# Kernel optimization log

Hardware: AMD Instinct MI355X
Metric: run time of the kernel (lower is better)

Reference implementation:

```python
import jax, jax.numpy as jnp
import numpy as np

DIM = 1024
HEAD_SIZE = 128
B, N = 4, 4096

def setup_inputs() -> dict:
    key = jax.random.key(0)
    kx, kq, kk, kv = jax.random.split(key, 4)
    s = (1.0 / DIM) ** 0.5  # ~ torch Linear init scale
    return {
        "x": jax.random.normal(kx, (B, N, DIM), dtype=jnp.float32),
        "Wq": jax.random.uniform(kq, (HEAD_SIZE, DIM), dtype=jnp.float32, minval=-s, maxval=s),
        "Wk": jax.random.uniform(kk, (HEAD_SIZE, DIM), dtype=jnp.float32, minval=-s, maxval=s),
        "Wv": jax.random.uniform(kv, (HEAD_SIZE, DIM), dtype=jnp.float32, minval=-s, maxval=s),
    }

def reference(x, Wq, Wk, Wv):
    # x: [B, N, dim]; W*: [head_size, dim] (torch Linear convention y = x @ W.T)
    q = jnp.einsum('bnd,hd->bnh', x, Wq)
    k = jnp.einsum('bnd,hd->bnh', x, Wk)
    v = jnp.einsum('bnd,hd->bnh', x, Wv)
    scale = DIM ** (-0.5)  # NOTE: original scales by dim**-0.5, not head_size
    scores = jnp.einsum('bnh,bmh->bnm', q, k) * scale  # [B, N, N]
    weights = jax.nn.softmax(scores, axis=-1)
    context = jnp.einsum('bnm,bmh->bnh', weights, v)  # [B, N, head_size]
    return context
```

## Files before the change

### kernel.cpp

```cpp
#include <hip/hip_runtime.h>

using bf16x8   = __attribute__((ext_vector_type(8))) __bf16;
using f32x4    = __attribute__((ext_vector_type(4))) float;
using f32x16   = __attribute__((ext_vector_type(16))) float;
using floatv4  = __attribute__((ext_vector_type(4))) float;
using ushortv4 = __attribute__((ext_vector_type(4))) unsigned short;
using ushortv8 = __attribute__((ext_vector_type(8))) unsigned short;
using uintv4   = __attribute__((ext_vector_type(4))) unsigned int;

#define N_SEQ 4096
#define N_B   4
#define DIMK  1024
#define HS    128
#define ROWS  (N_B * N_SEQ)
#define KVB   32
#define TT    (N_SEQ / KVB)
#define CEXPF 0.045084220027780106f

__device__ __forceinline__ unsigned short f2bf(float f) {
    unsigned u = __builtin_bit_cast(unsigned, f);
    u += 0x7FFFu + ((u >> 16) & 1u);
    return (unsigned short)(u >> 16);
}

__device__ __forceinline__ unsigned cvtpk(float lo, float hi) {
    unsigned r;
    asm("v_cvt_pk_bf16_f32 %0, %1, %2" : "=v"(r) : "v"(lo), "v"(hi));
    return r;
}

__device__ __forceinline__ void gload16(const unsigned short* g, unsigned short* l) {
    __builtin_amdgcn_global_load_lds(
        (const __attribute__((address_space(1))) unsigned int*)g,
        (__attribute__((address_space(3))) unsigned int*)l, 16, 0, 0);
}

__global__ __launch_bounds__(256) void castw_kernel(
    const float* __restrict__ Wq,
    const float* __restrict__ Wk,
    const float* __restrict__ Wv,
    unsigned short* __restrict__ Wb)
{
    const int blk = blockIdx.x;
    const int z = blk >> 6;
    const float* src = (z == 0) ? Wq : (z == 1) ? Wk : Wv;
    unsigned short* dst = Wb + (size_t)z * (HS * DIMK);
    size_t i = (size_t)(blk & 63) * 2048 + (size_t)threadIdx.x * 8;
    floatv4 a = *reinterpret_cast<const floatv4*>(src + i);
    floatv4 b = *reinterpret_cast<const floatv4*>(src + i + 4);
    ushortv8 o = { f2bf(a.x), f2bf(a.y), f2bf(a.z), f2bf(a.w),
                   f2bf(b.x), f2bf(b.y), f2bf(b.z), f2bf(b.w) };
    *reinterpret_cast<ushortv8*>(dst + i) = o;
}

__global__ __launch_bounds__(256, 3) void proj_kernel(
    const float* __restrict__ X,
    const unsigned short* __restrict__ Wb,
    unsigned short* __restrict__ Qb,
    unsigned short* __restrict__ Kb,
    unsigned short* __restrict__ Vt)
{
    const int z = blockIdx.y;
    const unsigned short* __restrict__ Wz = Wb + (size_t)z * (HS * DIMK);
    const int row0 = blockIdx.x * 64;
    __shared__ unsigned short smem[2 * 64 * 64 + 2 * 128 * 64];
    unsigned short* Xs0 = smem;
    unsigned short* Ws0 = smem + 2 * 64 * 64;
    const int tid = threadIdx.x;
    const int wv = tid >> 6, lane = tid & 63;
    const int lr = lane & 15, lg = lane >> 4;

    const int xrow = tid >> 2, xc = (tid & 3) * 16;
    const float* xg = X + (size_t)(row0 + xrow) * DIMK + xc;
    const int xs0 = (tid & 3) * 2;
    floatv4 xr[4];

    f32x4 acc[4][2] = {};

    auto loadX = [&](int k0) {
        #pragma unroll
        for (int i = 0; i < 4; ++i)
            xr[i] = *reinterpret_cast<const floatv4*>(xg + k0 + i * 4);
    };
    auto writeX = [&](int buf) {
        uintv4 w0 = { cvtpk(xr[0].x, xr[0].y), cvtpk(xr[0].z, xr[0].w),
                      cvtpk(xr[1].x, xr[1].y), cvtpk(xr[1].z, xr[1].w) };
        uintv4 w1 = { cvtpk(xr[2].x, xr[2].y), cvtpk(xr[2].z, xr[2].w),
                      cvtpk(xr[3].x, xr[3].y), cvtpk(xr[3].z, xr[3].w) };
        unsigned short* xb = Xs0 + buf * (64 * 64) + xrow * 64;
        *reinterpret_cast<uintv4*>(&xb[((xs0 ^ (xrow & 7)) * 8)]) = w0;
        *reinterpret_cast<uintv4*>(&xb[(((xs0 + 1) ^ (xrow & 7)) * 8)]) = w1;
    };
    auto stageW = [&](int buf, int k0) {
        #pragma unroll
        for (int i = 0; i < 4; ++i) {
            int g = wv * 4 + i;
            int r = g * 8 + (lane >> 3);
            int sp = (lane & 7) ^ (r & 7);
            gload16(Wz + (size_t)r * DIMK + k0 + sp * 8,
                    Ws0 + buf * (128 * 64) + g * 8 * 64);
        }
    };

    loadX(0);
    stageW(0, 0);
    asm volatile("s_waitcnt vmcnt(0)" ::: "memory");
    writeX(0);
    __syncthreads();

    for (int ks = 0; ks < DIMK / 64; ++ks) {
        const int cur = ks & 1;
        const bool more = (ks + 1 < DIMK / 64);
        if (more) { loadX((ks + 1) * 64); stageW(cur ^ 1, (ks + 1) * 64); }

        const unsigned short* Xc = Xs0 + cur * (64 * 64);
        const unsigned short* Wc = Ws0 + cur * (128 * 64);
        bf16x8 af[4][2], bfr[2][2];
        #pragma unroll
        for (int mi = 0; mi < 4; ++mi)
            #pragma unroll
            for (int kk = 0; kk < 2; ++kk)
                af[mi][kk] = *reinterpret_cast<const bf16x8*>(
                    &Xc[(mi * 16 + lr) * 64 + (((kk * 4 + lg) ^ (lr & 7)) * 8)]);
        #pragma unroll
        for (int ni = 0; ni < 2; ++ni)
            #pragma unroll
            for (int kk = 0; kk < 2; ++kk)
                bfr[ni][kk] = *reinterpret_cast<const bf16x8*>(
                    &Wc[(wv * 32 + ni * 16 + lr) * 64 + (((kk * 4 + lg) ^ (lr & 7)) * 8)]);
        #pragma unroll
        for (int kk = 0; kk < 2; ++kk)
            #pragma unroll
            for (int mi = 0; mi < 4; ++mi)
                #pragma unroll
                for (int ni = 0; ni < 2; ++ni)
                    acc[mi][ni] = __builtin_amdgcn_mfma_f32_16x16x32_bf16(
                        af[mi][kk], bfr[ni][kk], acc[mi][ni], 0, 0, 0);

        if (more) {
            asm volatile("s_waitcnt vmcnt(0)" ::: "memory");
            writeX(cur ^ 1);
        }
        __syncthreads();
    }

    if (z < 2) {
        unsigned short* O = (z == 0) ? Qb : Kb;
        const float qs = (z == 0) ? CEXPF : 1.0f;
        #pragma unroll
        for (int mi = 0; mi < 4; ++mi) {
            int rowb = row0 + mi * 16 + lg * 4;
            #pragma unroll
            for (int ni = 0; ni < 2; ++ni) {
                int col = wv * 32 + ni * 16 + lr;
                #pragma unroll
                for (int r = 0; r < 4; ++r)
                    O[(size_t)(rowb + r) * HS + col] = f2bf(acc[mi][ni][r] * qs);
            }
        }
    } else {
        unsigned short* Cs = smem;
        #pragma unroll
        for (int mi = 0; mi < 4; ++mi)
            #pragma unroll
            for (int ni = 0; ni < 2; ++ni)
                #pragma unroll
                for (int r = 0; r < 4; ++r)
                    Cs[(mi * 16 + lg * 4 + r) * 136 + wv * 32 + ni * 16 + lr] = f2bf(acc[mi][ni][r]);
        __syncthreads();
        const int b  = row0 >> 12;
        const int n0 = row0 & (N_SEQ - 1);
        #pragma unroll
        for (int i = 0; i < 2; ++i) {
            int idx = tid + i * 256;
            int d = idx >> 2, c8 = idx & 3;
            ushortv8 v;
            #pragma unroll
            for (int j = 0; j < 8; ++j)
                v[j] = Cs[(c8 * 8 + j) * 136 + d];
            *reinterpret_cast<ushortv8*>(Vt + (size_t)b * HS * N_SEQ + (size_t)d * N_SEQ + n0 + c8 * 8) = v;
        }
        #pragma unroll
        for (int i = 0; i < 2; ++i) {
            int idx = tid + i * 256;
            int d = idx >> 2, c8 = (idx & 3) + 4;
            ushortv8 v;
            #pragma unroll
            for (int j = 0; j < 8; ++j)
                v[j] = Cs[(c8 * 8 + j) * 136 + d];
            *reinterpret_cast<ushortv8*>(Vt + (size_t)b * HS * N_SEQ + (size_t)d * N_SEQ + n0 + c8 * 8) = v;
        }
    }
}

__global__ __launch_bounds__(256, 3) void attn_kernel(
    const unsigned short* __restrict__ Qb,
    const unsigned short* __restrict__ Kb,
    const unsigned short* __restrict__ Vt,
    unsigned short* __restrict__ part,
    float* __restrict__ plsum,
    int S)
{
    int qblk, split;
    {
        const int bid = blockIdx.x;
        if (S == 6) {
            const int chunk = bid >> 8, rem = bid & 255;
            const int member = rem >> 3, xcd = rem & 7;
            const int g = chunk * 8 + xcd;
            const int b = g / 6;
            split = g - b * 6;
            qblk = b * 32 + member;
        } else {
            qblk = bid & 127;
            split = bid >> 7;
        }
    }
    const int tid = threadIdx.x;
    const int wv = tid >> 6, lane = tid & 63;
    const int l31 = lane & 31, h = lane >> 5;
    const int b    = qblk >> 5;
    const int row0 = (qblk & 31) * 128 + wv * 32;

    __shared__ unsigned short Ks[3][KVB * 128];
    __shared__ unsigned short Vs[3][128 * KVB];

    bf16x8 qf[8];
    {
        const unsigned short* qp = Qb + ((size_t)b * N_SEQ + row0 + l31) * HS + h * 8;
        #pragma unroll
        for (int kk = 0; kk < 8; ++kk)
            qf[kk] = *reinterpret_cast<const bf16x8*>(qp + kk * 16);
    }

    const int base = TT / S, rem = TT % S;
    const int nt = base + (split < rem ? 1 : 0);
    const int kv_begin = (split * base + (split < rem ? split : rem)) * KVB;

    const unsigned short* Kbb = Kb + (size_t)b * N_SEQ * HS;
    const unsigned short* Vbb = Vt + (size_t)b * HS * N_SEQ;

    auto stage = [&](int buf, int kv0) {
        #pragma unroll
        for (int i = 0; i < 2; ++i) {
            int g = wv * 2 + i;
            int r = g * 4 + (lane >> 4);
            int sp = (lane & 15) ^ (r & 7);
            gload16(Kbb + (size_t)(kv0 + r) * HS + sp * 8, &Ks[buf][g * 4 * 128]);
        }
        #pragma unroll
        for (int i = 0; i < 2; ++i) {
            int g = wv * 2 + i;
            int r = g * 16 + (lane >> 2);
            int sp = (lane & 3) ^ ((r >> 1) & 3);
            gload16(Vbb + (size_t)r * N_SEQ + kv0 + sp * 8, &Vs[buf][g * 16 * KVB]);
        }
    };

    f32x16 ctx[4] = {};
    float lsum = 0.f;

    stage(0, kv_begin);
    stage(1, kv_begin + KVB);
    int cur = 0, nxt = 2;
    for (int t = 0; t < nt; ++t) {
        if (t + 2 < nt) {
            asm volatile("s_waitcnt vmcnt(4)\n\ts_barrier" ::: "memory");
            stage(nxt, kv_begin + (t + 2) * KVB);
        } else if (t + 1 < nt) {
            asm volatile("s_waitcnt vmcnt(4)\n\ts_barrier" ::: "memory");
        } else {
            asm volatile("s_waitcnt vmcnt(0)\n\ts_barrier" ::: "memory");
        }

        f32x16 st0 = {}, st1 = {};
        __builtin_amdgcn_s_setprio(1);
        #pragma unroll
        for (int kk = 0; kk < 8; kk += 2) {
            bf16x8 kf0 = *reinterpret_cast<const bf16x8*>(
                &Ks[cur][l31 * 128 + (((kk * 2 + h) ^ (l31 & 7)) * 8)]);
            st0 = __builtin_amdgcn_mfma_f32_32x32x16_bf16(kf0, qf[kk], st0, 0, 0, 0);
            bf16x8 kf1 = *reinterpret_cast<const bf16x8*>(
                &Ks[cur][l31 * 128 + ((((kk + 1) * 2 + h) ^ (l31 & 7)) * 8)]);
            st1 = __builtin_amdgcn_mfma_f32_32x32x16_bf16(kf1, qf[kk + 1], st1, 0, 0, 0);
        }
        __builtin_amdgcn_s_setprio(0);

        float p[16];
        #pragma unroll
        for (int r = 0; r < 16; ++r)
            p[r] = __builtin_amdgcn_exp2f(st0[r] + st1[r]);

        {
            float a0 = (p[0] + p[1])   + (p[2] + p[3]);
            float a1 = (p[4] + p[5])   + (p[6] + p[7]);
            float a2 = (p[8] + p[9])   + (p[10] + p[11]);
            float a3 = (p[12] + p[13]) + (p[14] + p[15]);
            lsum += (a0 + a1) + (a2 + a3);
        }

        bf16x8 pf[2];
        #pragma unroll
        for (int half = 0; half < 2; ++half) {
            unsigned a  = cvtpk(p[half*8 + 0], p[half*8 + 1]);
            unsigned bq = cvtpk(p[half*8 + 2], p[half*8 + 3]);
            unsigned c  = cvtpk(p[half*8 + 4], p[half*8 + 5]);
            unsigned d  = cvtpk(p[half*8 + 6], p[half*8 + 7]);
            asm("v_permlane32_swap_b32 %0, %1" : "+v"(a), "+v"(c));
            asm("v_permlane32_swap_b32 %0, %1" : "+v"(bq), "+v"(d));
            uintv4 w = { a, bq, c, d };
            pf[half] = __builtin_bit_cast(bf16x8, w);
        }

        __builtin_amdgcn_s_setprio(1);
        #pragma unroll
        for (int dt = 0; dt < 4; ++dt) {
            int d = dt * 32 + l31;
            bf16x8 vf0 = *reinterpret_cast<const bf16x8*>(
                &Vs[cur][d * KVB + (((0 + h) ^ ((d >> 1) & 3)) * 8)]);
            ctx[dt] = __builtin_amdgcn_mfma_f32_32x32x16_bf16(pf[0], vf0, ctx[dt], 0, 0, 0);
            bf16x8 vf1 = *reinterpret_cast<const bf16x8*>(
                &Vs[cur][d * KVB + (((2 + h) ^ ((d >> 1) & 3)) * 8)]);
            ctx[dt] = __builtin_amdgcn_mfma_f32_32x32x16_bf16(pf[1], vf1, ctx[dt], 0, 0, 0);
        }
        __builtin_amdgcn_s_setprio(0);

        cur = (cur == 2) ? 0 : cur + 1;
        nxt = (nxt == 2) ? 0 : nxt + 1;
    }

    lsum += __shfl_xor(lsum, 32);

    const int qt = qblk * 4 + wv;
    unsigned short* pp = part + ((size_t)qt * S + split) * (32 * 128);
    #pragma unroll
    for (int rp = 0; rp < 4; ++rp)
        #pragma unroll
        for (int rq = 0; rq < 4; ++rq) {
            const int r = rp * 4 + rq;
            const int q = rq + 8 * rp + 4 * h;
            #pragma unroll
            for (int dt = 0; dt < 4; ++dt)
                pp[q * 128 + dt * 32 + l31] = (unsigned short)(cvtpk(ctx[dt][r], ctx[dt][r]) & 0xFFFFu);
        }
    if (h == 0)
        plsum[((size_t)qt * S + split) * 32 + l31] = lsum;
}

__global__ __launch_bounds__(256) void reduce_kernel(
    const unsigned short* __restrict__ part,
    const float* __restrict__ plsum,
    float* __restrict__ out, int S)
{
    const int id = blockIdx.x * 256 + threadIdx.x;
    const int d4 = (id & 31) * 4;
    const int grow = id >> 5;
    const int qt = grow >> 5, q = grow & 31;
    f32x4 c = {0.f, 0.f, 0.f, 0.f};
    float l = 0.f;
    for (int s = 0; s < S; ++s) {
        ushortv4 pv = *reinterpret_cast<const ushortv4*>(
            &part[(((size_t)qt * S + s) * 32 + q) * 128 + d4]);
        #pragma unroll
        for (int j = 0; j < 4; ++j)
            c[j] += __builtin_bit_cast(float, (unsigned)pv[j] << 16);
        l += plsum[((size_t)qt * S + s) * 32 + q];
    }
    float inv = 1.0f / l;
    f32x4 o = { c[0]*inv, c[1]*inv, c[2]*inv, c[3]*inv };
    *reinterpret_cast<f32x4*>(&out[(size_t)grow * 128 + d4]) = o;
}

extern "C" void kernel_launch(void* const* d_in, const int* in_sizes, int n_in,
                              void* d_out, int out_size, void* d_ws, size_t ws_size,
                              hipStream_t stream) {
    const float* x  = (const float*)d_in[0];
    const float* wq = (const float*)d_in[1];
    const float* wk = (const float*)d_in[2];
    const float* wv = (const float*)d_in[3];

    unsigned short* Wb = (unsigned short*)d_ws;
    unsigned short* Qb = Wb + (size_t)3 * HS * DIMK;
    unsigned short* Kb = Qb + (size_t)ROWS * HS;
    unsigned short* Vt = Kb + (size_t)ROWS * HS;
    float* plsum = (float*)(Vt + (size_t)N_B * HS * N_SEQ);

    const size_t fixed = (size_t)3 * HS * DIMK * 2 + (size_t)3 * ROWS * HS * 2;
    const size_t per_split = (size_t)512 * 32 * 4 + (size_t)512 * 32 * 128 * 2;

    int S;
    if      (ws_size >= fixed + 6 * per_split) S = 6;
    else if (ws_size >= fixed + 4 * per_split) S = 4;
    else if (ws_size >= fixed + 2 * per_split) S = 2;
    else                                       S = 1;

    unsigned short* part = (unsigned short*)(plsum + (size_t)512 * S * 32);

    castw_kernel<<<192, 256, 0, stream>>>(wq, wk, wv, Wb);
    proj_kernel<<<dim3(256, 3), 256, 0, stream>>>(x, Wb, Qb, Kb, Vt);
    attn_kernel<<<dim3(128 * S), 256, 0, stream>>>(Qb, Kb, Vt, part, plsum, S);
    reduce_kernel<<<(ROWS * HS) / 1024, 256, 0, stream>>>(part, plsum, (float*)d_out, S);
}
```

Before: 83.22 us.

## Stage fp32 X directly to LDS with triple-buffered async loads in projection

The projection kernel now loads fp32 X tiles straight into shared memory with global_load_lds instead of going through registers, and converts them to bf16 when reading fragments from LDS. The K loop changes from 64-wide double buffering to 32-wide triple buffering, using a partial vmcnt wait and a single barrier per step so that two stages of loads stay in flight. This is meant to take the register round-trip and the full vmcnt(0) stall off the critical path. The cost is twice as many iterations and barriers, plus the fp32-to-bf16 conversion being redone by every wave that reads the same X tile.

```diff
diff --git a/kernel.cpp b/kernel.cpp
--- a/kernel.cpp
+++ b/kernel.cpp
@@ -29,7 +29,7 @@
     return r;
 }
 
-__device__ __forceinline__ void gload16(const unsigned short* g, unsigned short* l) {
+__device__ __forceinline__ void gload16(const void* g, void* l) {
     __builtin_amdgcn_global_load_lds(
         (const __attribute__((address_space(1))) unsigned int*)g,
         (__attribute__((address_space(3))) unsigned int*)l, 16, 0, 0);
@@ -63,87 +63,80 @@
     const int z = blockIdx.y;
     const unsigned short* __restrict__ Wz = Wb + (size_t)z * (HS * DIMK);
     const int row0 = blockIdx.x * 64;
-    __shared__ unsigned short smem[2 * 64 * 64 + 2 * 128 * 64];
-    unsigned short* Xs0 = smem;
-    unsigned short* Ws0 = smem + 2 * 64 * 64;
+    __shared__ unsigned short smem[3 * (4096 + 4096)];
     const int tid = threadIdx.x;
     const int wv = tid >> 6, lane = tid & 63;
     const int lr = lane & 15, lg = lane >> 4;
 
-    const int xrow = tid >> 2, xc = (tid & 3) * 16;
-    const float* xg = X + (size_t)(row0 + xrow) * DIMK + xc;
-    const int xs0 = (tid & 3) * 2;
-    floatv4 xr[4];
+    const int xR  = (lane >> 3);
+    const int xP  = lane & 7;
+    const int wR  = (lane >> 2);
+    const int wP  = lane & 3;
+
+    auto stage = [&](int buf, int ks) {
+        unsigned short* base = smem + buf * 8192;
+        #pragma unroll
+        for (int i = 0; i < 2; ++i) {
+            int r = wv * 16 + i * 8 + xR;
+            int sl = xP ^ (r & 7);
+            gload16(X + (size_t)(row0 + r) * DIMK + ks * 32 + sl * 4,
+                    base + (size_t)(wv * 16 + i * 8) * 64);
+        }
+        #pragma unroll
+        for (int i = 0; i < 2; ++i) {
+            int r = wv * 32 + i * 16 + wR;
+            int sl = wP ^ ((r >> 1) & 3);
+            gload16(Wz + (size_t)r * DIMK + ks * 32 + sl * 8,
+                    base + 4096 + (size_t)(wv * 32 + i * 16) * 32);
+        }
+    };
 
     f32x4 acc[4][2] = {};
 
-    auto loadX = [&](int k0) {
-        #pragma unroll
-        for (int i = 0; i < 4; ++i)
-            xr[i] = *reinterpret_cast<const floatv4*>(xg + k0 + i * 4);
-    };
-    auto writeX = [&](int buf) {
-        uintv4 w0 = { cvtpk(xr[0].x, xr[0].y), cvtpk(xr[0].z, xr[0].w),
-                      cvtpk(xr[1].x, xr[1].y), cvtpk(xr[1].z, xr[1].w) };
-        uintv4 w1 = { cvtpk(xr[2].x, xr[2].y), cvtpk(xr[2].z, xr[2].w),
-                      cvtpk(xr[3].x, xr[3].y), cvtpk(xr[3].z, xr[3].w) };
-        unsigned short* xb = Xs0 + buf * (64 * 64) + xrow * 64;
-        *reinterpret_cast<uintv4*>(&xb[((xs0 ^ (xrow & 7)) * 8)]) = w0;
-        *reinterpret_cast<uintv4*>(&xb[(((xs0 + 1) ^ (xrow & 7)) * 8)]) = w1;
-    };
-    auto stageW = [&](int buf, int k0) {
-        #pragma unroll
-        for (int i = 0; i < 4; ++i) {
-            int g = wv * 4 + i;
-            int r = g * 8 + (lane >> 3);
-            int sp = (lane & 7) ^ (r & 7);
-            gload16(Wz + (size_t)r * DIMK + k0 + sp * 8,
-                    Ws0 + buf * (128 * 64) + g * 8 * 64);
-        }
-    };
-
-    loadX(0);
-    stageW(0, 0);
-    asm volatile("s_waitcnt vmcnt(0)" ::: "memory");
-    writeX(0);
+    stage(0, 0);
+    stage(1, 1);
+    for (int t = 0; t < 32; ++t) {
+        if (t + 1 < 32)
+            asm volatile("s_waitcnt vmcnt(4)\n\ts_barrier" ::: "memory");
+        else
+            asm volatile("s_waitcnt vmcnt(0)\n\ts_barrier" ::: "memory");
+        if (t + 2 < 32) {
+            int nb = t + 2; nb -= (nb / 3) * 3;
+            stage(nb, t + 2);
+        }
+
+        const int cur = t - (t / 3) * 3;
+        const float* Xc = reinterpret_cast<const float*>(smem + cur * 8192);
+        const unsigned short* Wc = smem + cur * 8192 + 4096;
+
+        bf16x8 af[4];
+        #pragma unroll
+        for (int mi = 0; mi < 4; ++mi) {
+            const int r = mi * 16 + lr;
+            f32x4 a = *reinterpret_cast<const f32x4*>(
+                &Xc[r * 32 + (((lg * 2)     ^ (lr & 7)) << 2)]);
+            f32x4 b = *reinterpret_cast<const f32x4*>(
+                &Xc[r * 32 + (((lg * 2 + 1) ^ (lr & 7)) << 2)]);
+            uintv4 w = { cvtpk(a.x, a.y), cvtpk(a.z, a.w),
+                         cvtpk(b.x, b.y), cvtpk(b.z, b.w) };
+            af[mi] = __builtin_bit_cast(bf16x8, w);
+        }
+        bf16x8 bfr[2];
+        #pragma unroll
+        for (int ni = 0; ni < 2; ++ni) {
+            const int wr = wv * 32 + ni * 16 + lr;
+            bfr[ni] = *reinterpret_cast<const bf16x8*>(
+                &Wc[wr * 32 + ((lg ^ ((wr >> 1) & 3)) * 8)]);
+        }
+        #pragma unroll
+        for (int mi = 0; mi < 4; ++mi)
+            #pragma unroll
+            for (int ni = 0; ni < 2; ++ni)
+                acc[mi][ni] = __builtin_amdgcn_mfma_f32_16x16x32_bf16(
+                    af[mi], bfr[ni], acc[mi][ni], 0, 0, 0);
+    }
+
     __syncthreads();
-
-    for (int ks = 0; ks < DIMK / 64; ++ks) {
-        const int cur = ks & 1;
-        const bool more = (ks + 1 < DIMK / 64);
-        if (more) { loadX((ks + 1) * 64); stageW(cur ^ 1, (ks + 1) * 64); }
-
-        const unsigned short* Xc = Xs0 + cur * (64 * 64);
-        const unsigned short* Wc = Ws0 + cur * (128 * 64);
-        bf16x8 af[4][2], bfr[2][2];
-        #pragma unroll
-        for (int mi = 0; mi < 4; ++mi)
-            #pragma unroll
-            for (int kk = 0; kk < 2; ++kk)
-                af[mi][kk] = *reinterpret_cast<const bf16x8*>(
-                    &Xc[(mi * 16 + lr) * 64 + (((kk * 4 + lg) ^ (lr & 7)) * 8)]);
-        #pragma unroll
-        for (int ni = 0; ni < 2; ++ni)
-            #pragma unroll
-            for (int kk = 0; kk < 2; ++kk)
-                bfr[ni][kk] = *reinterpret_cast<const bf16x8*>(
-                    &Wc[(wv * 32 + ni * 16 + lr) * 64 + (((kk * 4 + lg) ^ (lr & 7)) * 8)]);
-        #pragma unroll
-        for (int kk = 0; kk < 2; ++kk)
-            #pragma unroll
-            for (int mi = 0; mi < 4; ++mi)
-                #pragma unroll
-                for (int ni = 0; ni < 2; ++ni)
-                    acc[mi][ni] = __builtin_amdgcn_mfma_f32_16x16x32_bf16(
-                        af[mi][kk], bfr[ni][kk], acc[mi][ni], 0, 0, 0);
-
-        if (more) {
-            asm volatile("s_waitcnt vmcnt(0)" ::: "memory");
-            writeX(cur ^ 1);
-        }
-        __syncthreads();
-    }
-
     if (z < 2) {
         unsigned short* O = (z == 0) ? Qb : Kb;
         const float qs = (z == 0) ? CEXPF : 1.0f;
@@ -205,12 +198,12 @@
     {
         const int bid = blockIdx.x;
         if (S == 6) {
-            const int chunk = bid >> 8, rem = bid & 255;
-            const int member = rem >> 3, xcd = rem & 7;
+            const int chunk = bid >> 8, r2 = bid & 255;
+            const int member = r2 >> 3, xcd = r2 & 7;
             const int g = chunk * 8 + xcd;
-            const int b = g / 6;
-            split = g - b * 6;
-            qblk = b * 32 + member;
+            const int bb = g / 6;
+            split = g - bb * 6;
+            qblk = bb * 32 + member;
         } else {
             qblk = bid & 127;
             split = bid >> 7;
```

New measurement: 84.76 us. About the same (+1.8%).
